# Kernel tuning notes

Hardware: AMD Instinct MI355X
Metric: run time of the kernel (lower is better)

## Reference

```python
import jax, jax.numpy as jnp
import numpy as np

N, E, ENC, EMB, PI = 100000, 1600000, 128, 128, 98
ALPHA1, ALPHA2 = 0.5, 0.5


def setup_inputs() -> dict:
    key = jax.random.key(0)
    ks = jax.random.split(key, 20)
    s = 0.05
    return {
        "x": jax.random.normal(ks[0], (N, ENC), jnp.float32),
        "d2an": jax.random.normal(ks[1], (N, PI), jnp.float32),
        "ei0": jax.random.randint(ks[2], (2, E), 0, N, jnp.int32),
        "ew0": jax.random.uniform(ks[3], (E,), jnp.float32, 0.1, 4.0),
        "ei1": jax.random.randint(ks[4], (2, E), 0, N, jnp.int32),
        "ew1": jax.random.uniform(ks[5], (E,), jnp.float32, 0.1, 4.0),
        "nodeW1": jax.random.normal(ks[6], (ENC, ENC + PI), jnp.float32) * s,
        "nodeW2": jax.random.normal(ks[7], (ENC, ENC + PI), jnp.float32) * s,
        "W1a": jax.random.normal(ks[8], (EMB, ENC), jnp.float32) * s,
        "W1b": jax.random.normal(ks[9], (EMB, ENC), jnp.float32) * s,
        "W2a": jax.random.normal(ks[10], (EMB, ENC), jnp.float32) * s,
        "W2b": jax.random.normal(ks[11], (EMB, ENC), jnp.float32) * s,
        "W3a": jax.random.normal(ks[12], (EMB, EMB), jnp.float32) * s,
        "W3b": jax.random.normal(ks[13], (EMB, EMB), jnp.float32) * s,
        "W4a": jax.random.normal(ks[14], (EMB, EMB), jnp.float32) * s,
        "W4b": jax.random.normal(ks[15], (EMB, EMB), jnp.float32) * s,
    }


def _layer(x, ei, ew, W1, W2, nodeW, d2an, first):
    """PosKnnGNNLayer.forward: add self loops, optional nodeLin, GCN deg norm +
    edge norm, gather -> lin1/lin2 -> scale -> scatter-add (aggr='add')."""
    n = x.shape[0]
    loop = jnp.arange(n, dtype=ei.dtype)
    row = jnp.concatenate([ei[0], loop])          # source nodes (x_j)
    col = jnp.concatenate([ei[1], loop])          # target nodes (aggregation)
    attr = jnp.concatenate([ew, jnp.ones((n,), ew.dtype)])  # self-loop fill=1.0
    if first:
        x = jnp.concatenate([x, d2an], axis=1) @ nodeW.T
    deg = jax.ops.segment_sum(jnp.ones_like(attr), col, num_segments=n)
    dis = jnp.where(deg > 0, jax.lax.rsqrt(jnp.maximum(deg, 1.0)), 0.0)
    deg_norm = dis[row] * dis[col]                # [E']
    einv = attr ** -0.5
    einv = jnp.where(jnp.isinf(einv), 0.0, einv)
    einv = jnp.minimum(einv, 1.0)                 # clamp >1 to 1
    h1 = x @ W1.T                                 # [N, out]
    h2 = x @ W2.T
    msg = deg_norm[:, None] * h1[row] + einv[:, None] * h2[row]  # [E', out]
    return jax.ops.segment_sum(msg, col, num_segments=n)


def reference(x, d2an, ei0, ew0, ei1, ew1, nodeW1, nodeW2,
              W1a, W1b, W2a, W2b, W3a, W3b, W4a, W4b):
    # eval mode: dropout(p=0.3) is identity
    x0 = jax.nn.relu(_layer(x, ei0, ew0, W1a, W1b, nodeW1, d2an, True))
    x1 = jax.nn.relu(_layer(x, ei1, ew1, W2a, W2b, nodeW2, d2an, True))
    xm = ALPHA1 * x0 + ALPHA2 * x1
    x0 = jax.nn.relu(_layer(xm, ei0, ew0, W3a, W3b, None, None, False))
    x1 = jax.nn.relu(_layer(xm, ei1, ew1, W4a, W4b, None, None, False))
    return ALPHA1 * x0 + ALPHA2 * x1
```

## Files before the change

### kernel.cpp

```cpp
#include <hip/hip_runtime.h>
#include <hip/hip_fp16.h>
#include <stdint.h>

#define NN 100000
#define NE 1600000
#define ETOT (NE + NN)

typedef __attribute__((ext_vector_type(8))) short bf16x8;
typedef __attribute__((ext_vector_type(4))) float f32x4;
typedef __attribute__((ext_vector_type(4))) unsigned short us4;

__device__ __forceinline__ float bf2f(unsigned short u) {
    union { unsigned int i; float f; } x; x.i = ((unsigned int)u) << 16; return x.f;
}
__device__ __forceinline__ unsigned short f2bf(float f) {
    union { float f; unsigned int i; } x; x.f = f;
    unsigned int i = x.i;
    return (unsigned short)((i + 0x7FFFu + ((i >> 16) & 1u)) >> 16);
}
__device__ __forceinline__ int packab(float a, float b) {
    unsigned int ua = __half_as_ushort(__float2half_rn(a));
    unsigned int ub = __half_as_ushort(__float2half_rn(b));
    return (int)(ua | (ub << 16));
}
__device__ __forceinline__ float2 unpackab(int p) {
    float a = __half2float(__ushort_as_half((unsigned short)(p & 0xFFFF)));
    float b = __half2float(__ushort_as_half((unsigned short)(((unsigned int)p) >> 16)));
    return make_float2(a, b);
}

__global__ void k_init_deg(int* deg0, int* deg1) {
    int i = blockIdx.x * 256 + threadIdx.x;
    if (i < NN) { deg0[i] = 1; deg1[i] = 1; }
}

__global__ void k_count(const int* col0, const int* col1, int* deg0, int* deg1) {
    int t = blockIdx.x * 256 + threadIdx.x;
    if (t * 4 >= NE) return;
    const int* col = blockIdx.y ? col1 : col0;
    int* deg = blockIdx.y ? deg1 : deg0;
    int4 a = ((const int4*)col)[t];
    atomicAdd(&deg[a.x], 1); atomicAdd(&deg[a.y], 1);
    atomicAdd(&deg[a.z], 1); atomicAdd(&deg[a.w], 1);
}

__global__ void k_scan1(const int* deg0, const int* deg1, int* rp0, int* rp1s, int* bsum) {
    __shared__ int s[256];
    const int* deg = blockIdx.y ? deg1 : deg0;
    int* rp = (blockIdx.y ? rp1s : rp0) + 1;
    int* bs = bsum + blockIdx.y * 128;
    int tid = threadIdx.x;
    int base = blockIdx.x * 1024 + tid * 4;
    int v0 = 0, v1 = 0, v2 = 0, v3 = 0;
    if (base + 0 < NN) v0 = deg[base + 0];
    if (base + 1 < NN) v1 = deg[base + 1];
    if (base + 2 < NN) v2 = deg[base + 2];
    if (base + 3 < NN) v3 = deg[base + 3];
    int sum = v0 + v1 + v2 + v3;
    s[tid] = sum; __syncthreads();
    for (int off = 1; off < 256; off <<= 1) {
        int t = (tid >= off) ? s[tid - off] : 0;
        __syncthreads(); s[tid] += t; __syncthreads();
    }
    int run = s[tid] - sum;
    if (base + 0 < NN) { run += v0; rp[base + 0] = run; }
    if (base + 1 < NN) { run += v1; rp[base + 1] = run; }
    if (base + 2 < NN) { run += v2; rp[base + 2] = run; }
    if (base + 3 < NN) { run += v3; rp[base + 3] = run; }
    if (tid == 255) bs[blockIdx.x] = s[255];
}

__global__ void k_scan2(int* bsum, int nb) {
    __shared__ int s[128];
    int* bs = bsum + blockIdx.x * 128;
    int tid = threadIdx.x;
    int v = (tid < nb) ? bs[tid] : 0;
    s[tid] = v; __syncthreads();
    for (int off = 1; off < 128; off <<= 1) {
        int t = (tid >= off) ? s[tid - off] : 0;
        __syncthreads(); s[tid] += t; __syncthreads();
    }
    if (tid < nb) bs[tid] = s[tid] - v;
}

__global__ void k_scan3(int* rp0, int* rp1s, const int* bsum) {
    int* rowptr = blockIdx.y ? rp1s : rp0;
    int add = bsum[blockIdx.y * 128 + blockIdx.x];
    int tid = threadIdx.x;
    int base = blockIdx.x * 1024 + tid * 4;
    #pragma unroll
    for (int i = 0; i < 4; i++) {
        int idx = base + i;
        if (idx < NN) rowptr[idx + 1] += add;
    }
    if (blockIdx.x == 0 && tid == 0) rowptr[0] = 0;
}

__global__ void k_self(const int* rp0, const int* rp1s, const int* deg0, const int* deg1,
                       int2* eo0, int2* eo1, int* cur0, int* cur1, float* dis0, float* dis1) {
    int i = blockIdx.x * 256 + threadIdx.x;
    if (i >= NN) return;
    const int* rowptr = blockIdx.y ? rp1s : rp0;
    const int* deg = blockIdx.y ? deg1 : deg0;
    int2* eo = blockIdx.y ? eo1 : eo0;
    int* cursor = blockIdx.y ? cur1 : cur0;
    float* dis = blockIdx.y ? dis1 : dis0;
    int p = rowptr[i];
    float d = (float)deg[i];
    eo[p] = make_int2(i, packab(1.0f / d, 1.0f));
    cursor[i] = p + 1;
    dis[i] = rsqrtf(d);
}

__global__ void k_fill(const int* ei0, const float* ew0, const int* ei1, const float* ew1,
                       int* cur0, int* cur1, const float* dis0, const float* dis1,
                       int2* eo0, int2* eo1) {
    int e = blockIdx.x * 256 + threadIdx.x;
    if (e >= NE) return;
    const int* er = blockIdx.y ? ei1 : ei0;
    const float* ew = blockIdx.y ? ew1 : ew0;
    int* cursor = blockIdx.y ? cur1 : cur0;
    const float* dis = blockIdx.y ? dis1 : dis0;
    int2* eo = blockIdx.y ? eo1 : eo0;
    int r = er[e], c = er[NE + e];
    float a = dis[r] * dis[c];
    float b = fminf(rsqrtf(ew[e]), 1.0f);
    int p = atomicAdd(&cursor[c], 1);
    eo[p] = make_int2(r, packab(a, b));
}

__global__ void k_packx(const float* x, const float* d2, unsigned short* Xc) {
    int idx = blockIdx.x * 256 + threadIdx.x;
    if (idx >= NN * 64) return;
    int r = idx >> 6, k4 = (idx & 63) << 2;
    us4 o;
    if (k4 < 128) {
        float4 v = *(const float4*)(x + (size_t)r * 128 + k4);
        o[0] = f2bf(v.x); o[1] = f2bf(v.y); o[2] = f2bf(v.z); o[3] = f2bf(v.w);
    } else {
        #pragma unroll
        for (int i = 0; i < 4; i++) {
            int k = k4 + i;
            float v = (k < 226) ? d2[(size_t)r * 98 + (k - 128)] : 0.f;
            o[i] = f2bf(v);
        }
    }
    *(us4*)(Xc + (size_t)r * 256 + k4) = o;
}

__global__ void k_packw(const float* wn1, const float* wn2,
                        const float* w1a, const float* w1b,
                        const float* w2a, const float* w2b,
                        const float* w3a, const float* w3b,
                        const float* w4a, const float* w4b,
                        unsigned short* Wfnode, unsigned short* WfL) {
    int idx = blockIdx.x * 256 + threadIdx.x;
    if (idx < 65536) {
        int j = idx & 7, lane = (idx >> 3) & 63, ct = (idx >> 9) & 15, ks = idx >> 13;
        int k = ks * 32 + (lane >> 4) * 8 + j;
        int c = ct * 16 + (lane & 15);
        float v = 0.f;
        if (k < 226) v = (c < 128) ? wn1[c * 226 + k] : wn2[(c - 128) * 226 + k];
        Wfnode[idx] = f2bf(v);
    } else if (idx < 196608) {
        int li = idx - 65536;
        int set = li >> 15, r = li & 32767;
        const float* wa = (set == 0) ? w1a : (set == 1) ? w2a : (set == 2) ? w3a : w4a;
        const float* wb = (set == 0) ? w1b : (set == 1) ? w2b : (set == 2) ? w3b : w4b;
        int j = r & 7, lane = (r >> 3) & 63, ct = (r >> 9) & 7, ks = r >> 12;
        int k = ks * 32 + (lane >> 4) * 8 + j;
        int c = ct * 16 + (lane & 15);
        float v = (k < 128) ? wa[c * 128 + k] : wb[c * 128 + (k - 128)];
        WfL[li] = f2bf(v);
    }
}

template <int SRST, int SOFF>
__global__ __launch_bounds__(256) void k_agg(const unsigned short* S,
                                             const int* rowptr, const int2* eg,
                                             unsigned short* G) {
    int c = blockIdx.x * 4 + (threadIdx.x >> 6);
    int lane = threadIdx.x & 63;
    if (c >= NN) return;
    float a0 = 0.f, a1 = 0.f, b0 = 0.f, b1 = 0.f;
    int jb = rowptr[c], je = rowptr[c + 1];
    const unsigned short* Sb = S + SOFF + lane * 2;
    int j = jb;
    for (; j + 16 <= je; j += 16) {
        int2 e[16]; unsigned int u[16];
        #pragma unroll
        for (int i = 0; i < 16; i++) e[i] = eg[j + i];
        #pragma unroll
        for (int i = 0; i < 16; i++)
            u[i] = *(const unsigned int*)(Sb + (size_t)e[i].x * SRST);
        #pragma unroll
        for (int i = 0; i < 16; i++) {
            float2 w = unpackab(e[i].y);
            float x0 = bf2f((unsigned short)(u[i] & 0xFFFF));
            float x1 = bf2f((unsigned short)(u[i] >> 16));
            a0 += w.x * x0; a1 += w.x * x1; b0 += w.y * x0; b1 += w.y * x1;
        }
    }
    for (; j + 4 <= je; j += 4) {
        int2 e[4]; unsigned int u[4];
        #pragma unroll
        for (int i = 0; i < 4; i++) e[i] = eg[j + i];
        #pragma unroll
        for (int i = 0; i < 4; i++)
            u[i] = *(const unsigned int*)(Sb + (size_t)e[i].x * SRST);
        #pragma unroll
        for (int i = 0; i < 4; i++) {
            float2 w = unpackab(e[i].y);
            float x0 = bf2f((unsigned short)(u[i] & 0xFFFF));
            float x1 = bf2f((unsigned short)(u[i] >> 16));
            a0 += w.x * x0; a1 += w.x * x1; b0 += w.y * x0; b1 += w.y * x1;
        }
    }
    for (; j < je; j++) {
        int2 e = eg[j];
        unsigned int u = *(const unsigned int*)(Sb + (size_t)e.x * SRST);
        float2 w = unpackab(e.y);
        float x0 = bf2f((unsigned short)(u & 0xFFFF));
        float x1 = bf2f((unsigned short)(u >> 16));
        a0 += w.x * x0; a1 += w.x * x1; b0 += w.y * x0; b1 += w.y * x1;
    }
    unsigned int* gd = (unsigned int*)(G + (size_t)c * 256);
    gd[lane]      = (unsigned int)f2bf(a0) | ((unsigned int)f2bf(a1) << 16);
    gd[64 + lane] = (unsigned int)f2bf(b0) | ((unsigned int)f2bf(b1) << 16);
}

template <int MODE>
__global__ __launch_bounds__(256) void k_gemm(const unsigned short* A, int arst,
                                              const unsigned short* Wf, int nct_total,
                                              unsigned short* outB, float* outF,
                                              const unsigned short* T, int orst) {
    int wave = threadIdx.x >> 6, lane = threadIdx.x & 63;
    int m = lane & 15, quad = lane >> 4;
    int row0 = blockIdx.x * 64 + wave * 16;
    int arow = row0 + m;
    bool rowok = arow < NN;
    const unsigned short* Ap = A + (size_t)arow * arst + quad * 8;
    int ctbase = blockIdx.y * 8;
    f32x4 acc[8];
    #pragma unroll
    for (int t = 0; t < 8; t++) acc[t] = (f32x4){0.f, 0.f, 0.f, 0.f};

    #pragma unroll
    for (int ks = 0; ks < 8; ks++) {
        bf16x8 a;
        if (rowok) a = *(const bf16x8*)(Ap + ks * 32);
        else       a = (bf16x8){0, 0, 0, 0, 0, 0, 0, 0};
        const unsigned short* wp = Wf + ((size_t)(ks * nct_total + ctbase) * 64 + lane) * 8;
        #pragma unroll
        for (int t = 0; t < 8; t++) {
            bf16x8 b = *(const bf16x8*)(wp + t * 512);
            acc[t] = __builtin_amdgcn_mfma_f32_16x16x32_bf16(a, b, acc[t], 0, 0, 0);
        }
    }

    int col0 = blockIdx.y * 128;
    #pragma unroll
    for (int t = 0; t < 8; t++) {
        int c = col0 + t * 16 + m;
        #pragma unroll
        for (int rg = 0; rg < 4; rg++) {
            int r = row0 + quad * 4 + rg;
            if (r < NN) {
                float v = acc[t][rg];
                if (MODE == 0) {
                    outB[(size_t)r * orst + c] = f2bf(v);
                } else {
                    float tv = bf2f(T[(size_t)r * 128 + c]);
                    float o = 0.5f * fmaxf(tv, 0.f) + 0.5f * fmaxf(v, 0.f);
                    if (MODE == 1) outB[(size_t)r * orst + c] = f2bf(o);
                    else           outF[(size_t)r * 128 + c] = o;
                }
            }
        }
    }
}

extern "C" void kernel_launch(void* const* d_in, const int* in_sizes, int n_in,
                              void* d_out, int out_size, void* d_ws, size_t ws_size,
                              hipStream_t stream) {
    const float* x      = (const float*)d_in[0];
    const float* d2an   = (const float*)d_in[1];
    const int*   ei0    = (const int*)d_in[2];
    const float* ew0    = (const float*)d_in[3];
    const int*   ei1    = (const int*)d_in[4];
    const float* ew1    = (const float*)d_in[5];
    const float* nodeW1 = (const float*)d_in[6];
    const float* nodeW2 = (const float*)d_in[7];
    const float* W1a = (const float*)d_in[8],  *W1b = (const float*)d_in[9];
    const float* W2a = (const float*)d_in[10], *W2b = (const float*)d_in[11];
    const float* W3a = (const float*)d_in[12], *W3b = (const float*)d_in[13];
    const float* W4a = (const float*)d_in[14], *W4b = (const float*)d_in[15];
    float* out = (float*)d_out;

    char* p = (char*)d_ws;
    auto alloc = [&](size_t bytes) -> char* {
        char* r = p; p += (bytes + 255) & ~(size_t)255; return r;
    };
    unsigned short* bufA   = (unsigned short*)alloc((size_t)NN * 256 * 2);
    unsigned short* bufB   = (unsigned short*)alloc((size_t)NN * 256 * 2);
    unsigned short* Tbuf   = (unsigned short*)alloc((size_t)NN * 128 * 2);
    unsigned short* Wfnode = (unsigned short*)alloc(65536 * 2);
    unsigned short* WfL    = (unsigned short*)alloc((size_t)4 * 32768 * 2);
    int*    deg0    = (int*)alloc((size_t)NN * 4);
    int*    deg1    = (int*)alloc((size_t)NN * 4);
    int*    rowptr0 = (int*)alloc((size_t)(NN + 1) * 4);
    int*    rowptr1 = (int*)alloc((size_t)(NN + 1) * 4);
    int*    cur0    = (int*)alloc((size_t)NN * 4);
    int*    cur1    = (int*)alloc((size_t)NN * 4);
    int*    bsum    = (int*)alloc(2 * 128 * 4);
    float*  dis0    = (float*)alloc((size_t)NN * 4);
    float*  dis1    = (float*)alloc((size_t)NN * 4);
    int2*   eo0     = (int2*)alloc((size_t)ETOT * 8);
    int2*   eo1     = (int2*)alloc((size_t)ETOT * 8);

    int nbN  = (NN + 255) / 256;
    int nbE1 = (NE + 255) / 256;
    int nbE4 = (NE / 4 + 255) / 256;
    int nbS  = (NN + 1023) / 1024;
    dim3 gP((NN + 63) / 64, 2);
    dim3 gL((NN + 63) / 64, 1);
    int nbA = (NN + 3) / 4;

    k_init_deg<<<nbN, 256, 0, stream>>>(deg0, deg1);
    k_count<<<dim3(nbE4, 2), 256, 0, stream>>>(ei0 + NE, ei1 + NE, deg0, deg1);
    k_scan1<<<dim3(nbS, 2), 256, 0, stream>>>(deg0, deg1, rowptr0, rowptr1, bsum);
    k_scan2<<<2, 128, 0, stream>>>(bsum, nbS);
    k_scan3<<<dim3(nbS, 2), 256, 0, stream>>>(rowptr0, rowptr1, bsum);
    k_self<<<dim3(nbN, 2), 256, 0, stream>>>(rowptr0, rowptr1, deg0, deg1,
                                             eo0, eo1, cur0, cur1, dis0, dis1);
    k_fill<<<dim3(nbE1, 2), 256, 0, stream>>>(ei0, ew0, ei1, ew1,
                                              cur0, cur1, dis0, dis1, eo0, eo1);

    k_packx<<<(NN * 64 + 255) / 256, 256, 0, stream>>>(x, d2an, bufA);
    k_packw<<<768, 256, 0, stream>>>(nodeW1, nodeW2, W1a, W1b, W2a, W2b,
                                     W3a, W3b, W4a, W4b, Wfnode, WfL);

    k_gemm<0><<<gP, 256, 0, stream>>>(bufA, 256, Wfnode, 16, bufB, nullptr, nullptr, 256);
    k_agg<256, 0><<<nbA, 256, 0, stream>>>(bufB, rowptr0, eo0, bufA);
    k_gemm<0><<<gL, 256, 0, stream>>>(bufA, 256, WfL, 8, Tbuf, nullptr, nullptr, 128);
    k_agg<256, 128><<<nbA, 256, 0, stream>>>(bufB, rowptr1, eo1, bufA);
    k_gemm<1><<<gL, 256, 0, stream>>>(bufA, 256, WfL + 32768, 8, bufB, nullptr, Tbuf, 128);

    k_agg<128, 0><<<nbA, 256, 0, stream>>>(bufB, rowptr0, eo0, bufA);
    k_gemm<0><<<gL, 256, 0, stream>>>(bufA, 256, WfL + 2 * 32768, 8, Tbuf, nullptr, nullptr, 128);
    k_agg<128, 0><<<nbA, 256, 0, stream>>>(bufB, rowptr1, eo1, bufA);
    k_gemm<2><<<gL, 256, 0, stream>>>(bufA, 256, WfL + 3 * 32768, 8, nullptr, out, Tbuf, 128);
}
```

Before: 958.0 us.

## Two-pass bucketed CSR fill to localize scattered edge writes

Replaces the single scatter pass that atomically appends each edge to its target node's CSR slot with two passes. The first pass bins edges into 128-node buckets using per-bucket atomic cursors and writes them to a staging area reused from bufB. The second pass places each bucket's edges into final per-node slots, where the writes stay within a small contiguous range. The goal is to turn random scattered 8-byte writes and atomics over the whole array into more local traffic, at the cost of an extra read and write pass plus heavy atomic contention on the bucket cursors.

```diff
diff --git a/kernel.cpp b/kernel.cpp
--- a/kernel.cpp
+++ b/kernel.cpp
@@ -5,6 +5,7 @@
 #define NN 100000
 #define NE 1600000
 #define ETOT (NE + NN)
+#define NBUCK ((NN + 127) >> 7)
 
 typedef __attribute__((ext_vector_type(8))) short bf16x8;
 typedef __attribute__((ext_vector_type(4))) float f32x4;
@@ -97,7 +98,8 @@
 }
 
 __global__ void k_self(const int* rp0, const int* rp1s, const int* deg0, const int* deg1,
-                       int2* eo0, int2* eo1, int* cur0, int* cur1, float* dis0, float* dis1) {
+                       int2* eo0, int2* eo1, int* cur0, int* cur1, float* dis0, float* dis1,
+                       int* bcur0, int* bcur1) {
     int i = blockIdx.x * 256 + threadIdx.x;
     if (i >= NN) return;
     const int* rowptr = blockIdx.y ? rp1s : rp0;
@@ -105,28 +107,51 @@
     int2* eo = blockIdx.y ? eo1 : eo0;
     int* cursor = blockIdx.y ? cur1 : cur0;
     float* dis = blockIdx.y ? dis1 : dis0;
+    int* bcur = blockIdx.y ? bcur1 : bcur0;
     int p = rowptr[i];
     float d = (float)deg[i];
     eo[p] = make_int2(i, packab(1.0f / d, 1.0f));
     cursor[i] = p + 1;
     dis[i] = rsqrtf(d);
-}
-
-__global__ void k_fill(const int* ei0, const float* ew0, const int* ei1, const float* ew1,
-                       int* cur0, int* cur1, const float* dis0, const float* dis1,
-                       int2* eo0, int2* eo1) {
+    if ((i & 127) == 0) bcur[i >> 7] = p;
+}
+
+__global__ void k_bucket(const int* ei0, const float* ew0, const int* ei1, const float* ew1,
+                         const float* dis0, const float* dis1,
+                         int* bcur0, int* bcur1, int2* st0, int2* st1) {
     int e = blockIdx.x * 256 + threadIdx.x;
     if (e >= NE) return;
     const int* er = blockIdx.y ? ei1 : ei0;
     const float* ew = blockIdx.y ? ew1 : ew0;
-    int* cursor = blockIdx.y ? cur1 : cur0;
     const float* dis = blockIdx.y ? dis1 : dis0;
-    int2* eo = blockIdx.y ? eo1 : eo0;
+    int* bcur = blockIdx.y ? bcur1 : bcur0;
+    int2* st = blockIdx.y ? st1 : st0;
     int r = er[e], c = er[NE + e];
     float a = dis[r] * dis[c];
     float b = fminf(rsqrtf(ew[e]), 1.0f);
-    int p = atomicAdd(&cursor[c], 1);
-    eo[p] = make_int2(r, packab(a, b));
+    int p = atomicAdd(&bcur[c >> 7], 1);
+    st[p] = make_int2(r | ((c & 127) << 17), packab(a, b));
+}
+
+__global__ __launch_bounds__(256) void k_place(const int* rp0, const int* rp1s,
+                        const int* bcur0, const int* bcur1,
+                        const int2* st0, const int2* st1,
+                        int* cur0, int* cur1, int2* eo0, int2* eo1) {
+    int b = blockIdx.x;
+    const int* rowptr = blockIdx.y ? rp1s : rp0;
+    const int* bcur = blockIdx.y ? bcur1 : bcur0;
+    const int2* st = blockIdx.y ? st1 : st0;
+    int* cur = blockIdx.y ? cur1 : cur0;
+    int2* eo = blockIdx.y ? eo1 : eo0;
+    int start = rowptr[b << 7];
+    int end = bcur[b];
+    for (int j = start + (int)threadIdx.x; j < end; j += 256) {
+        int2 rec = st[j];
+        int r = rec.x & 0x1FFFF;
+        int c = (b << 7) + ((rec.x >> 17) & 0x7F);
+        int p = atomicAdd(&cur[c], 1);
+        eo[p] = make_int2(r, rec.y);
+    }
 }
 
 __global__ void k_packx(const float* x, const float* d2, unsigned short* Xc) {
@@ -317,6 +342,11 @@
     float*  dis1    = (float*)alloc((size_t)NN * 4);
     int2*   eo0     = (int2*)alloc((size_t)ETOT * 8);
     int2*   eo1     = (int2*)alloc((size_t)ETOT * 8);
+    int*    bcur0   = (int*)alloc((size_t)NBUCK * 4);
+    int*    bcur1   = (int*)alloc((size_t)NBUCK * 4);
+
+    int2* st0 = (int2*)bufB;
+    int2* st1 = st0 + ETOT;
 
     int nbN  = (NN + 255) / 256;
     int nbE1 = (NE + 255) / 256;
@@ -332,9 +362,12 @@
     k_scan2<<<2, 128, 0, stream>>>(bsum, nbS);
     k_scan3<<<dim3(nbS, 2), 256, 0, stream>>>(rowptr0, rowptr1, bsum);
     k_self<<<dim3(nbN, 2), 256, 0, stream>>>(rowptr0, rowptr1, deg0, deg1,
-                                             eo0, eo1, cur0, cur1, dis0, dis1);
-    k_fill<<<dim3(nbE1, 2), 256, 0, stream>>>(ei0, ew0, ei1, ew1,
-                                              cur0, cur1, dis0, dis1, eo0, eo1);
+                                             eo0, eo1, cur0, cur1, dis0, dis1,
+                                             bcur0, bcur1);
+    k_bucket<<<dim3(nbE1, 2), 256, 0, stream>>>(ei0, ew0, ei1, ew1,
+                                                dis0, dis1, bcur0, bcur1, st0, st1);
+    k_place<<<dim3(NBUCK, 2), 256, 0, stream>>>(rowptr0, rowptr1, bcur0, bcur1,
+                                                st0, st1, cur0, cur1, eo0, eo1);
 
     k_packx<<<(NN * 64 + 255) / 256, 256, 0, stream>>>(x, d2an, bufA);
     k_packw<<<768, 256, 0, stream>>>(nodeW1, nodeW2, W1a, W1b, W2a, W2b,
```

New measurement: 1.521 ms. +58.7%, slower.
